# Kernel optimization log

Measured on AMD Instinct MI355X. Metric: run time of the kernel, lower is better.

Reference implementation:

```python
import jax, jax.numpy as jnp
import numpy as np
from jax import lax

# NLM hyperparameters (from init_kwargs)
H_PARAM = 7.0 / 255.0          # OpenCV h is in 0-255 intensity units; images are in [0,1]
H2 = H_PARAM * H_PARAM
T = 7                          # template (patch) window size
TH = T // 2
S = 21                         # search window size
SH = S // 2


def setup_inputs() -> dict:
    key = jax.random.key(0)
    x = jax.random.uniform(key, (4, 1, 1024, 1024), dtype=jnp.float32)
    return {"x": x}


def _box_mean(d):
    # mean filter over TxT template window with reflect ('same') padding,
    # done as two separable 1D convolutions.
    k = (jnp.ones((T,), dtype=d.dtype) / T)
    dp = jnp.pad(d, ((0, 0), (0, 0), (TH, TH), (TH, TH)), mode="reflect")
    dn = ("NCHW", "OIHW", "NCHW")
    y = lax.conv_general_dilated(dp, k.reshape(1, 1, T, 1), (1, 1), "VALID", dimension_numbers=dn)
    y = lax.conv_general_dilated(y, k.reshape(1, 1, 1, T), (1, 1), "VALID", dimension_numbers=dn)
    return y


def reference(x):
    B, C, H, W = x.shape
    xc = jnp.clip(x, 0.0, 1.0)
    # reflect-pad by the search radius so every shift is a plain slice
    padded = jnp.pad(xc, ((0, 0), (0, 0), (SH, SH), (SH, SH)), mode="reflect")

    # all SxS = 441 search-window offsets, as padded-array slice origins in [0, 2*SH]
    oy, ox = jnp.meshgrid(jnp.arange(S, dtype=jnp.int32), jnp.arange(S, dtype=jnp.int32), indexing="ij")
    offsets = jnp.stack([oy.reshape(-1), ox.reshape(-1)], axis=-1)  # [441, 2]

    zero = jnp.int32(0)

    def body(carry, off):
        wsum, vsum = carry
        shifted = lax.dynamic_slice(padded, (zero, zero, off[0], off[1]), (B, C, H, W))
        dist = _box_mean((xc - shifted) ** 2)          # mean squared patch difference
        w = jnp.exp(-dist / H2)                        # NLM similarity weight
        return (wsum + w, vsum + w * shifted), None

    init = (jnp.zeros_like(xc), jnp.zeros_like(xc))
    (wsum, vsum), _ = lax.scan(body, init, offsets)
    out = vsum / wsum
    return jnp.clip(out, 0.0, 1.0)
```

## Files before the change

### kernel.cpp

```cpp
#include <hip/hip_runtime.h>
#include <cstddef>


constexpr int TS    = 32;
constexpr int XSTR  = 61;
constexpr int XROWS = 59;
constexpr int XSZ   = XROWS * XSTR;
constexpr int VT    = 33;
constexpr int VCOLS = 38;
constexpr int VS_SZ = VCOLS * VT;

__device__ __forceinline__ int refl(int i, int n) {
    i = (i < 0) ? -i : i;
    return (i >= n) ? (2 * n - 2 - i) : i;
}

template<bool FAST>
__device__ __forceinline__ void nlm_body(const float* __restrict__ img,
                                         float* __restrict__ out,
                                         int H, int W, int gx0, int gy0,
                                         float* __restrict__ xs,
                                         float* __restrict__ vsh, int tid)
{
    for (int e = tid; e < XSZ; e += 256) {
        int i = e / XSTR, j = e - i * XSTR;
        int jj = (j > 57) ? 57 : j;
        int gy = refl(gy0 - 13 + i, H);
        int gx = refl(gx0 - 13 + jj, W);
        float v = img[(size_t)gy * W + gx];
        xs[e] = fminf(fmaxf(v, 0.0f), 1.0f);
    }
    __syncthreads();

    const bool bv = (tid < 114);
    float u[17];
    int   aB = 0;
    int   aS[17];
    int   wb = 0;
    {
        int t  = bv ? tid : 0;
        int g  = t / 38;
        int cc = t - g * 38;
        int r  = g * 11;
        int mxm10 = refl(gx0 + cc - 3, W) - gx0 + 3;
        if constexpr (FAST) {
            aB = r * XSTR + mxm10;
#pragma unroll
            for (int i = 0; i < 17; ++i)
                u[i] = xs[(r + i + 10) * XSTR + mxm10 + 10];
        } else {
#pragma unroll
            for (int i = 0; i < 17; ++i) {
                int my = refl(gy0 + r + i - 3, H) - gy0 + 13;
                u[i]  = xs[my * XSTR + mxm10 + 10];
                aS[i] = (my - 10) * XSTR + mxm10;
            }
        }
        wb = cc * VT + r;
    }

    const bool cact = (tid >= 128);
    const int ct = cact ? (tid - 128) : 0;
    const int py = ct >> 2;
    const int c8 = (ct & 3) * 8;
    const int vb = c8 * VT + py;
    int svC = (py + 3) * XSTR + (c8 + 3);

    int oxB = 0;
    int oxC = 0;

    float ws[8], ac[8];
#pragma unroll
    for (int k = 0; k < 8; ++k) { ws[k] = 0.f; ac[k] = 0.f; }
    const float K = -(65025.0f / 2401.0f) * 1.4426950408889634f;
    const float HSKIP = 3.95f;

    auto bv_step = [&](int buf) {
        if (bv) {
            float* vo = vsh + buf * VS_SZ + wb;
            float q[17];
            if constexpr (FAST) {
#pragma unroll
                for (int i = 0; i < 17; ++i)
                    q[i] = xs[aB + i * XSTR];
            } else {
#pragma unroll
                for (int i = 0; i < 17; ++i)
                    q[i] = xs[aS[i]];
            }
#pragma unroll
            for (int i = 0; i < 17; ++i) {
                float d = u[i] - q[i];
                q[i] = d * d;
            }
            float s[11];
            s[0] = ((q[0] + q[1]) + (q[2] + q[3])) + ((q[4] + q[5]) + q[6]);
#pragma unroll
            for (int k = 1; k < 11; ++k)
                s[k] = s[k - 1] + (q[k + 6] - q[k - 1]);
#pragma unroll
            for (int k = 0; k < 11; ++k)
                vo[k] = s[k];
            if constexpr (FAST) {
                aB += (oxB == 20) ? (XSTR - 20) : 1;
            } else {
                int step = (oxB == 20) ? (XSTR - 20) : 1;
#pragma unroll
                for (int i = 0; i < 17; ++i) aS[i] += step;
            }
        }
        oxB = (oxB == 20) ? 0 : (oxB + 1);
    };

    auto c_step = [&](int buf) {
        if (cact) {
            const float* vp = vsh + buf * VS_SZ + vb;
            float v0  = vp[0],       v1  = vp[VT],      v2  = vp[2 * VT];
            float v3  = vp[3 * VT],  v4  = vp[4 * VT],  v5  = vp[5 * VT];
            float v6  = vp[6 * VT],  v7  = vp[7 * VT],  v8  = vp[8 * VT];
            float v9  = vp[9 * VT],  v10 = vp[10 * VT], v11 = vp[11 * VT];
            float v12 = vp[12 * VT], v13 = vp[13 * VT];
            float h0 = ((v0 + v1) + (v2 + v3)) + ((v4 + v5) + v6);
            float h1 = h0 - v0 + v7;
            float h2 = h1 - v1 + v8;
            float h3 = h2 - v2 + v9;
            float h4 = h3 - v3 + v10;
            float h5 = h4 - v4 + v11;
            float h6 = h5 - v5 + v12;
            float h7 = h6 - v6 + v13;
            float m = fminf(fminf(fminf(h0, h1), fminf(h2, h3)),
                            fminf(fminf(h4, h5), fminf(h6, h7)));
            if (__builtin_expect(__ballot(m <= HSKIP) != 0ull, 0)) {
                const int sp = svC + oxC;
                float x0 = xs[sp],     x1 = xs[sp + 1];
                float x2 = xs[sp + 2], x3 = xs[sp + 3];
                float x4 = xs[sp + 4], x5 = xs[sp + 5];
                float x6 = xs[sp + 6], x7 = xs[sp + 7];
                float w;
                w = __builtin_amdgcn_exp2f(h0 * K); ws[0] += w; ac[0] = fmaf(w, x0, ac[0]);
                w = __builtin_amdgcn_exp2f(h1 * K); ws[1] += w; ac[1] = fmaf(w, x1, ac[1]);
                w = __builtin_amdgcn_exp2f(h2 * K); ws[2] += w; ac[2] = fmaf(w, x2, ac[2]);
                w = __builtin_amdgcn_exp2f(h3 * K); ws[3] += w; ac[3] = fmaf(w, x3, ac[3]);
                w = __builtin_amdgcn_exp2f(h4 * K); ws[4] += w; ac[4] = fmaf(w, x4, ac[4]);
                w = __builtin_amdgcn_exp2f(h5 * K); ws[5] += w; ac[5] = fmaf(w, x5, ac[5]);
                w = __builtin_amdgcn_exp2f(h6 * K); ws[6] += w; ac[6] = fmaf(w, x6, ac[6]);
                w = __builtin_amdgcn_exp2f(h7 * K); ws[7] += w; ac[7] = fmaf(w, x7, ac[7]);
            }
        }
        if (oxC == 20) { oxC = 0; svC += XSTR; } else { ++oxC; }
    };

    bv_step(0);
    __syncthreads();
#pragma unroll 1
    for (int i = 1; i < 441; ++i) {
        bv_step(i & 1);
        c_step(1 - (i & 1));
        __syncthreads();
    }
    c_step(0);

    if (cact) {
        float4 oA, oB;
        oA.x = fminf(fmaxf(ac[0] * __builtin_amdgcn_rcpf(ws[0]), 0.f), 1.f);
        oA.y = fminf(fmaxf(ac[1] * __builtin_amdgcn_rcpf(ws[1]), 0.f), 1.f);
        oA.z = fminf(fmaxf(ac[2] * __builtin_amdgcn_rcpf(ws[2]), 0.f), 1.f);
        oA.w = fminf(fmaxf(ac[3] * __builtin_amdgcn_rcpf(ws[3]), 0.f), 1.f);
        oB.x = fminf(fmaxf(ac[4] * __builtin_amdgcn_rcpf(ws[4]), 0.f), 1.f);
        oB.y = fminf(fmaxf(ac[5] * __builtin_amdgcn_rcpf(ws[5]), 0.f), 1.f);
        oB.z = fminf(fmaxf(ac[6] * __builtin_amdgcn_rcpf(ws[6]), 0.f), 1.f);
        oB.w = fminf(fmaxf(ac[7] * __builtin_amdgcn_rcpf(ws[7]), 0.f), 1.f);
        float* op = &out[((size_t)blockIdx.z * H + (gy0 + py)) * W + (gx0 + c8)];
        *reinterpret_cast<float4*>(op)     = oA;
        *reinterpret_cast<float4*>(op + 4) = oB;
    }
}

__global__ __launch_bounds__(256)
void nlm_kernel(const float* __restrict__ img_all, float* __restrict__ out,
                int H, int W) {
    __shared__ __align__(16) float xs[XSZ];
    __shared__ __align__(16) float vsh[2 * VS_SZ];
    const int tid = threadIdx.x;
    const int gx0 = blockIdx.x * TS;
    const int gy0 = blockIdx.y * TS;
    const float* img = img_all + (size_t)blockIdx.z * H * W;
    if (gy0 - 3 >= 0 && gy0 + 35 < H)
        nlm_body<true>(img, out, H, W, gx0, gy0, xs, vsh, tid);
    else
        nlm_body<false>(img, out, H, W, gx0, gy0, xs, vsh, tid);
}

extern "C" void kernel_launch(void* const* d_in, const int* in_sizes, int n_in,
                              void* d_out, int out_size, void* d_ws, size_t ws_size,
                              hipStream_t stream) {
    const float* x = (const float*)d_in[0];
    float* out = (float*)d_out;
    const int H = 1024, W = 1024;
    const int B = in_sizes[0] / (H * W);
    dim3 grid(W / TS, H / TS, B);
    nlm_kernel<<<grid, dim3(256), 0, stream>>>(x, out, H, W);
}
```

Before: 862.6 us.

## Process two horizontal search offsets per pipeline step with packed float2 arithmetic

Each row of 21 search offsets is now handled as ten pairs plus one single, so a loop iteration covers two offsets and the number of block-wide barriers is roughly halved. The vertical box-sum producers compute two offsets at once using 2-wide float vectors, which can map to packed FP32 instructions, and store float2 into a shared buffer that is now twice as large. The consumers read float2 values and run the skip test and exp-accumulate separately for each offset. In exchange it uses more LDS and registers, which may lower occupancy, and every iteration pays a modulo-based branch to choose between the pair and single paths.

```diff
diff --git a/kernel.cpp b/kernel.cpp
--- a/kernel.cpp
+++ b/kernel.cpp
@@ -1,6 +1,8 @@
 #include <hip/hip_runtime.h>
 #include <cstddef>
 
+
+typedef float v2f __attribute__((ext_vector_type(2)));
 
 constexpr int TS    = 32;
 constexpr int XSTR  = 61;
@@ -20,7 +22,7 @@
                                          float* __restrict__ out,
                                          int H, int W, int gx0, int gy0,
                                          float* __restrict__ xs,
-                                         float* __restrict__ vsh, int tid)
+                                         v2f* __restrict__ vsh, int tid)
 {
     for (int e = tid; e < XSZ; e += 256) {
         int i = e / XSTR, j = e - i * XSTR;
@@ -65,8 +67,6 @@
     const int c8 = (ct & 3) * 8;
     const int vb = c8 * VT + py;
     int svC = (py + 3) * XSTR + (c8 + 3);
-
-    int oxB = 0;
     int oxC = 0;
 
     float ws[8], ac[8];
@@ -75,25 +75,23 @@
     const float K = -(65025.0f / 2401.0f) * 1.4426950408889634f;
     const float HSKIP = 3.95f;
 
-    auto bv_step = [&](int buf) {
+    auto bv_pair = [&](int buf) {
         if (bv) {
-            float* vo = vsh + buf * VS_SZ + wb;
-            float q[17];
-            if constexpr (FAST) {
-#pragma unroll
-                for (int i = 0; i < 17; ++i)
-                    q[i] = xs[aB + i * XSTR];
-            } else {
-#pragma unroll
-                for (int i = 0; i < 17; ++i)
-                    q[i] = xs[aS[i]];
-            }
-#pragma unroll
-            for (int i = 0; i < 17; ++i) {
-                float d = u[i] - q[i];
+            v2f* vo = vsh + buf * VS_SZ + wb;
+            v2f q[17];
+#pragma unroll
+            for (int i = 0; i < 17; ++i) {
+                int a = FAST ? (aB + i * XSTR) : aS[i];
+                v2f t; t.x = xs[a]; t.y = xs[a + 1];
+                q[i] = t;
+            }
+#pragma unroll
+            for (int i = 0; i < 17; ++i) {
+                v2f uu; uu.x = u[i]; uu.y = u[i];
+                v2f d = uu - q[i];
                 q[i] = d * d;
             }
-            float s[11];
+            v2f s[11];
             s[0] = ((q[0] + q[1]) + (q[2] + q[3])) + ((q[4] + q[5]) + q[6]);
 #pragma unroll
             for (int k = 1; k < 11; ++k)
@@ -102,24 +100,101 @@
             for (int k = 0; k < 11; ++k)
                 vo[k] = s[k];
             if constexpr (FAST) {
-                aB += (oxB == 20) ? (XSTR - 20) : 1;
+                aB += 2;
             } else {
-                int step = (oxB == 20) ? (XSTR - 20) : 1;
-#pragma unroll
-                for (int i = 0; i < 17; ++i) aS[i] += step;
-            }
-        }
-        oxB = (oxB == 20) ? 0 : (oxB + 1);
-    };
-
-    auto c_step = [&](int buf) {
+#pragma unroll
+                for (int i = 0; i < 17; ++i) aS[i] += 2;
+            }
+        }
+    };
+
+    auto bv_single = [&](int buf) {
+        if (bv) {
+            v2f* vo = vsh + buf * VS_SZ + wb;
+            float q[17];
+#pragma unroll
+            for (int i = 0; i < 17; ++i)
+                q[i] = xs[FAST ? (aB + i * XSTR) : aS[i]];
+#pragma unroll
+            for (int i = 0; i < 17; ++i) {
+                float d = u[i] - q[i];
+                q[i] = d * d;
+            }
+            float s[11];
+            s[0] = ((q[0] + q[1]) + (q[2] + q[3])) + ((q[4] + q[5]) + q[6]);
+#pragma unroll
+            for (int k = 1; k < 11; ++k)
+                s[k] = s[k - 1] + (q[k + 6] - q[k - 1]);
+#pragma unroll
+            for (int k = 0; k < 11; ++k) {
+                v2f t; t.x = s[k]; t.y = 0.0f;
+                vo[k] = t;
+            }
+            if constexpr (FAST) {
+                aB += XSTR - 20;
+            } else {
+#pragma unroll
+                for (int i = 0; i < 17; ++i) aS[i] += XSTR - 20;
+            }
+        }
+    };
+
+    auto c_pair = [&](int buf) {
         if (cact) {
-            const float* vp = vsh + buf * VS_SZ + vb;
-            float v0  = vp[0],       v1  = vp[VT],      v2  = vp[2 * VT];
-            float v3  = vp[3 * VT],  v4  = vp[4 * VT],  v5  = vp[5 * VT];
-            float v6  = vp[6 * VT],  v7  = vp[7 * VT],  v8  = vp[8 * VT];
-            float v9  = vp[9 * VT],  v10 = vp[10 * VT], v11 = vp[11 * VT];
-            float v12 = vp[12 * VT], v13 = vp[13 * VT];
+            const v2f* vp = vsh + buf * VS_SZ + vb;
+            v2f v0  = vp[0],       v1  = vp[VT],      v2  = vp[2 * VT];
+            v2f v3  = vp[3 * VT],  v4  = vp[4 * VT],  v5  = vp[5 * VT];
+            v2f v6  = vp[6 * VT],  v7  = vp[7 * VT],  v8  = vp[8 * VT];
+            v2f v9  = vp[9 * VT],  v10 = vp[10 * VT], v11 = vp[11 * VT];
+            v2f v12 = vp[12 * VT], v13 = vp[13 * VT];
+            v2f h0 = ((v0 + v1) + (v2 + v3)) + ((v4 + v5) + v6);
+            v2f h1 = h0 - v0 + v7;
+            v2f h2 = h1 - v1 + v8;
+            v2f h3 = h2 - v2 + v9;
+            v2f h4 = h3 - v3 + v10;
+            v2f h5 = h4 - v4 + v11;
+            v2f h6 = h5 - v5 + v12;
+            v2f h7 = h6 - v6 + v13;
+            float mx = fminf(fminf(fminf(h0.x, h1.x), fminf(h2.x, h3.x)),
+                             fminf(fminf(h4.x, h5.x), fminf(h6.x, h7.x)));
+            if (__builtin_expect(__ballot(mx <= HSKIP) != 0ull, 0)) {
+                const int sp = svC + oxC;
+                float w;
+                w = __builtin_amdgcn_exp2f(h0.x * K); ws[0] += w; ac[0] = fmaf(w, xs[sp],     ac[0]);
+                w = __builtin_amdgcn_exp2f(h1.x * K); ws[1] += w; ac[1] = fmaf(w, xs[sp + 1], ac[1]);
+                w = __builtin_amdgcn_exp2f(h2.x * K); ws[2] += w; ac[2] = fmaf(w, xs[sp + 2], ac[2]);
+                w = __builtin_amdgcn_exp2f(h3.x * K); ws[3] += w; ac[3] = fmaf(w, xs[sp + 3], ac[3]);
+                w = __builtin_amdgcn_exp2f(h4.x * K); ws[4] += w; ac[4] = fmaf(w, xs[sp + 4], ac[4]);
+                w = __builtin_amdgcn_exp2f(h5.x * K); ws[5] += w; ac[5] = fmaf(w, xs[sp + 5], ac[5]);
+                w = __builtin_amdgcn_exp2f(h6.x * K); ws[6] += w; ac[6] = fmaf(w, xs[sp + 6], ac[6]);
+                w = __builtin_amdgcn_exp2f(h7.x * K); ws[7] += w; ac[7] = fmaf(w, xs[sp + 7], ac[7]);
+            }
+            float my_ = fminf(fminf(fminf(h0.y, h1.y), fminf(h2.y, h3.y)),
+                              fminf(fminf(h4.y, h5.y), fminf(h6.y, h7.y)));
+            if (__builtin_expect(__ballot(my_ <= HSKIP) != 0ull, 0)) {
+                const int sp = svC + oxC + 1;
+                float w;
+                w = __builtin_amdgcn_exp2f(h0.y * K); ws[0] += w; ac[0] = fmaf(w, xs[sp],     ac[0]);
+                w = __builtin_amdgcn_exp2f(h1.y * K); ws[1] += w; ac[1] = fmaf(w, xs[sp + 1], ac[1]);
+                w = __builtin_amdgcn_exp2f(h2.y * K); ws[2] += w; ac[2] = fmaf(w, xs[sp + 2], ac[2]);
+                w = __builtin_amdgcn_exp2f(h3.y * K); ws[3] += w; ac[3] = fmaf(w, xs[sp + 3], ac[3]);
+                w = __builtin_amdgcn_exp2f(h4.y * K); ws[4] += w; ac[4] = fmaf(w, xs[sp + 4], ac[4]);
+                w = __builtin_amdgcn_exp2f(h5.y * K); ws[5] += w; ac[5] = fmaf(w, xs[sp + 5], ac[5]);
+                w = __builtin_amdgcn_exp2f(h6.y * K); ws[6] += w; ac[6] = fmaf(w, xs[sp + 6], ac[6]);
+                w = __builtin_amdgcn_exp2f(h7.y * K); ws[7] += w; ac[7] = fmaf(w, xs[sp + 7], ac[7]);
+            }
+        }
+        oxC += 2;
+    };
+
+    auto c_single = [&](int buf) {
+        if (cact) {
+            const v2f* vp = vsh + buf * VS_SZ + vb;
+            float v0  = vp[0].x,       v1  = vp[VT].x,      v2  = vp[2 * VT].x;
+            float v3  = vp[3 * VT].x,  v4  = vp[4 * VT].x,  v5  = vp[5 * VT].x;
+            float v6  = vp[6 * VT].x,  v7  = vp[7 * VT].x,  v8  = vp[8 * VT].x;
+            float v9  = vp[9 * VT].x,  v10 = vp[10 * VT].x, v11 = vp[11 * VT].x;
+            float v12 = vp[12 * VT].x, v13 = vp[13 * VT].x;
             float h0 = ((v0 + v1) + (v2 + v3)) + ((v4 + v5) + v6);
             float h1 = h0 - v0 + v7;
             float h2 = h1 - v1 + v8;
@@ -132,33 +207,31 @@
                             fminf(fminf(h4, h5), fminf(h6, h7)));
             if (__builtin_expect(__ballot(m <= HSKIP) != 0ull, 0)) {
                 const int sp = svC + oxC;
-                float x0 = xs[sp],     x1 = xs[sp + 1];
-                float x2 = xs[sp + 2], x3 = xs[sp + 3];
-                float x4 = xs[sp + 4], x5 = xs[sp + 5];
-                float x6 = xs[sp + 6], x7 = xs[sp + 7];
                 float w;
-                w = __builtin_amdgcn_exp2f(h0 * K); ws[0] += w; ac[0] = fmaf(w, x0, ac[0]);
-                w = __builtin_amdgcn_exp2f(h1 * K); ws[1] += w; ac[1] = fmaf(w, x1, ac[1]);
-                w = __builtin_amdgcn_exp2f(h2 * K); ws[2] += w; ac[2] = fmaf(w, x2, ac[2]);
-                w = __builtin_amdgcn_exp2f(h3 * K); ws[3] += w; ac[3] = fmaf(w, x3, ac[3]);
-                w = __builtin_amdgcn_exp2f(h4 * K); ws[4] += w; ac[4] = fmaf(w, x4, ac[4]);
-                w = __builtin_amdgcn_exp2f(h5 * K); ws[5] += w; ac[5] = fmaf(w, x5, ac[5]);
-                w = __builtin_amdgcn_exp2f(h6 * K); ws[6] += w; ac[6] = fmaf(w, x6, ac[6]);
-                w = __builtin_amdgcn_exp2f(h7 * K); ws[7] += w; ac[7] = fmaf(w, x7, ac[7]);
-            }
-        }
-        if (oxC == 20) { oxC = 0; svC += XSTR; } else { ++oxC; }
-    };
-
-    bv_step(0);
+                w = __builtin_amdgcn_exp2f(h0 * K); ws[0] += w; ac[0] = fmaf(w, xs[sp],     ac[0]);
+                w = __builtin_amdgcn_exp2f(h1 * K); ws[1] += w; ac[1] = fmaf(w, xs[sp + 1], ac[1]);
+                w = __builtin_amdgcn_exp2f(h2 * K); ws[2] += w; ac[2] = fmaf(w, xs[sp + 2], ac[2]);
+                w = __builtin_amdgcn_exp2f(h3 * K); ws[3] += w; ac[3] = fmaf(w, xs[sp + 3], ac[3]);
+                w = __builtin_amdgcn_exp2f(h4 * K); ws[4] += w; ac[4] = fmaf(w, xs[sp + 4], ac[4]);
+                w = __builtin_amdgcn_exp2f(h5 * K); ws[5] += w; ac[5] = fmaf(w, xs[sp + 5], ac[5]);
+                w = __builtin_amdgcn_exp2f(h6 * K); ws[6] += w; ac[6] = fmaf(w, xs[sp + 6], ac[6]);
+                w = __builtin_amdgcn_exp2f(h7 * K); ws[7] += w; ac[7] = fmaf(w, xs[sp + 7], ac[7]);
+            }
+        }
+        oxC = 0; svC += XSTR;
+    };
+
+    bv_pair(0);
     __syncthreads();
 #pragma unroll 1
-    for (int i = 1; i < 441; ++i) {
-        bv_step(i & 1);
-        c_step(1 - (i & 1));
+    for (int r = 1; r < 231; ++r) {
+        int m  = r % 11;
+        int pm = (r - 1) % 11;
+        if (m == 10) bv_single(r & 1); else bv_pair(r & 1);
+        if (pm == 10) c_single(1 - (r & 1)); else c_pair(1 - (r & 1));
         __syncthreads();
     }
-    c_step(0);
+    c_single(0);
 
     if (cact) {
         float4 oA, oB;
@@ -180,7 +253,7 @@
 void nlm_kernel(const float* __restrict__ img_all, float* __restrict__ out,
                 int H, int W) {
     __shared__ __align__(16) float xs[XSZ];
-    __shared__ __align__(16) float vsh[2 * VS_SZ];
+    __shared__ __align__(16) v2f vsh[2 * VS_SZ];
     const int tid = threadIdx.x;
     const int gx0 = blockIdx.x * TS;
     const int gy0 = blockIdx.y * TS;
```

Result: slower. 1.110 ms (+28.7%).
